# Kernel optimization log

Hardware: AMD Instinct MI355X
Metric: run time of the kernel (lower is better)

## Reference

```python
import jax, jax.numpy as jnp
import numpy as np

EPS = 1e-5


def setup_inputs() -> dict:
    key = jax.random.key(0)
    k1, k2, k3 = jax.random.split(key, 3)
    B, C, H, W = 32, 512, 56, 56
    R = 16
    x = jax.random.normal(k1, (B, C, H, W), dtype=jnp.float32)
    # SE excitation weights (no bias): Linear(C -> C//R), Linear(C//R -> C)
    w1 = jax.random.normal(k2, (C // R, C), dtype=jnp.float32) * (1.0 / np.sqrt(C))
    w2 = jax.random.normal(k3, (C, C // R), dtype=jnp.float32) * (1.0 / np.sqrt(C // R))
    # BatchNorm2d affine params (init: weight=1, bias=0)
    bn_weight = jnp.ones((C,), dtype=jnp.float32)
    bn_bias = jnp.zeros((C,), dtype=jnp.float32)
    return {"x": x, "w1": w1, "w2": w2, "bn_weight": bn_weight, "bn_bias": bn_bias}


def reference(x, w1, w2, bn_weight, bn_bias):
    B, C, H, W = x.shape
    # squeeze: global average pool -> [B, C]
    s = jnp.mean(x, axis=(2, 3))
    # excitation: Linear -> ReLU -> Linear -> Sigmoid
    e = jax.nn.sigmoid(jax.nn.relu(s @ w1.T) @ w2.T)  # [B, C]
    # scale
    y = x * e[:, :, None, None]  # [B, C, H, W]
    # BatchNorm2d (training-mode batch statistics, biased variance)
    mean = jnp.mean(y, axis=(0, 2, 3))
    var = jnp.var(y, axis=(0, 2, 3))
    yn = (y - mean[None, :, None, None]) * (
        bn_weight[None, :, None, None] * jax.lax.rsqrt(var + EPS)[None, :, None, None]
    ) + bn_bias[None, :, None, None]
    # unsqueeze dim=1 (c1=1) then rearrange 'b c1 (c2 c3) h w -> b c2 (c1 c3) h w', c2=2
    z = yn.reshape(B, 2, C // 2, H, W)
    # flatten(-2).mean(-1): mean over spatial dims -> [B, 2, C//2]
    z = jnp.mean(z, axis=(3, 4))
    # sum over dim=1 -> [B, C//2]
    return jnp.sum(z, axis=1)
```

## Files before the change

### kernel.cpp

```cpp
#include <hip/hip_runtime.h>
#include <math.h>

constexpr int B  = 32;
constexpr int C  = 512;
constexpr int CR = 32;
constexpr int HW = 56 * 56;
constexpr int NV4 = HW / 4;
constexpr float EPS = 1e-5f;

typedef float f32x4 __attribute__((ext_vector_type(4)));

__device__ inline f32x4 ntload(const f32x4* p) {
    return __builtin_nontemporal_load(p);
}

__global__ __launch_bounds__(256) void rowstats(const float* __restrict__ x,
                                                float* __restrict__ s_out,
                                                float* __restrict__ q_out) {
    const int wid  = threadIdx.x >> 6;
    const int lane = threadIdx.x & 63;
    const int row  = blockIdx.x * 4 + wid;
    const f32x4* xp = reinterpret_cast<const f32x4*>(x) + (size_t)row * NV4 + lane;
    float s = 0.f, q = 0.f;
    #pragma unroll
    for (int i = 0; i < 12; ++i) {
        f32x4 v = ntload(xp + i * 64);
        s += (v.x + v.y) + (v.z + v.w);
        q += (v.x * v.x + v.y * v.y) + (v.z * v.z + v.w * v.w);
    }
    {
        const float v = __builtin_nontemporal_load(x + (size_t)row * HW + 3072 + lane);
        s += v;
        q = fmaf(v, v, q);
    }
    #pragma unroll
    for (int off = 32; off > 0; off >>= 1) {
        s += __shfl_down(s, off, 64);
        q += __shfl_down(q, off, 64);
    }
    if (lane == 0) {
        s_out[row] = s * (1.0f / (float)HW);
        q_out[row] = q;
    }
}

__global__ __launch_bounds__(512) void excite(const float* __restrict__ s_in,
                                              const float* __restrict__ q_in,
                                              const float* __restrict__ w1,
                                              const float* __restrict__ w2,
                                              float* __restrict__ m_out,
                                              float* __restrict__ eq_out) {
    const int b   = blockIdx.x;
    const int tid = threadIdx.x;
    __shared__ __align__(16) float sh_s[C];
    __shared__ float sh_h[CR];

    const int j = tid >> 4, t = tid & 15;

    float4 w1r[8];
    {
        const float4* wr = reinterpret_cast<const float4*>(w1 + j * C);
        #pragma unroll
        for (int k = 0; k < 8; ++k) w1r[k] = wr[t + 16 * k];
    }
    float4 w2r[8];
    {
        const float4* w2p = reinterpret_cast<const float4*>(w2 + tid * CR);
        #pragma unroll
        for (int k = 0; k < 8; ++k) w2r[k] = w2p[k];
    }
    const float qv = q_in[b * C + tid];
    const float sv = s_in[b * C + tid];
    sh_s[tid] = sv;
    __syncthreads();

    {
        const float4* sr = reinterpret_cast<const float4*>(sh_s);
        float acc = 0.f;
        #pragma unroll
        for (int k = 0; k < 8; ++k) {
            float4 wv = w1r[k];
            float4 svv = sr[t + 16 * k];
            acc = fmaf(svv.x, wv.x, fmaf(svv.y, wv.y, fmaf(svv.z, wv.z, fmaf(svv.w, wv.w, acc))));
        }
        #pragma unroll
        for (int off = 8; off > 0; off >>= 1)
            acc += __shfl_down(acc, off, 16);
        if (t == 0) sh_h[j] = fmaxf(acc, 0.f);
    }
    __syncthreads();

    {
        const float4* hp = reinterpret_cast<const float4*>(sh_h);
        float acc = 0.f;
        #pragma unroll
        for (int k = 0; k < CR / 4; ++k) {
            float4 wv = w2r[k];
            float4 hv = hp[k];
            acc = fmaf(hv.x, wv.x, fmaf(hv.y, wv.y, fmaf(hv.z, wv.z, fmaf(hv.w, wv.w, acc))));
        }
        const float e = 1.0f / (1.0f + expf(-acc));
        m_out[b * C + tid]  = e * sv;
        eq_out[b * C + tid] = e * e * qv;
    }
}

__global__ __launch_bounds__(512) void bnout(const float* __restrict__ m_in,
                                             const float* __restrict__ eq_in,
                                             const float* __restrict__ bnw,
                                             const float* __restrict__ bnb,
                                             float* __restrict__ out) {
    const int c = threadIdx.x;
    __shared__ float sh_z[B][C / 2];
    const float wv = bnw[c];
    const float bv = bnb[c];
    float mv[B];
    float mean = 0.f, eq = 0.f;
    #pragma unroll
    for (int b = 0; b < B; ++b) {
        mv[b] = m_in[b * C + c];
        eq   += eq_in[b * C + c];
        mean += mv[b];
    }
    mean *= (1.0f / (float)B);
    const float var = eq * (1.0f / ((float)B * (float)HW)) - mean * mean;
    const float g   = wv * rsqrtf(var + EPS);

    if (c < C / 2) {
        #pragma unroll
        for (int b = 0; b < B; ++b)
            sh_z[b][c] = (mv[b] - mean) * g + bv;
    }
    __syncthreads();
    if (c >= C / 2) {
        const int c2 = c - C / 2;
        #pragma unroll
        for (int b = 0; b < B; ++b)
            out[b * (C / 2) + c2] = sh_z[b][c2] + ((mv[b] - mean) * g + bv);
    }
}

extern "C" void kernel_launch(void* const* d_in, const int* in_sizes, int n_in,
                              void* d_out, int out_size, void* d_ws, size_t ws_size,
                              hipStream_t stream) {
    const float* x   = (const float*)d_in[0];
    const float* w1  = (const float*)d_in[1];
    const float* w2  = (const float*)d_in[2];
    const float* bnw = (const float*)d_in[3];
    const float* bnb = (const float*)d_in[4];
    float* out = (float*)d_out;

    float* s_ws  = (float*)d_ws;
    float* q_ws  = s_ws + B * C;
    float* m_ws  = q_ws + B * C;
    float* eq_ws = m_ws + B * C;

    rowstats<<<dim3(B * C / 4), dim3(256), 0, stream>>>(x, s_ws, q_ws);
    excite<<<dim3(B), dim3(512), 0, stream>>>(s_ws, q_ws, w1, w2, m_ws, eq_ws);
    bnout<<<dim3(1), dim3(512), 0, stream>>>(m_ws, eq_ws, bnw, bnb, out);
}
```

Before: 40.31 us.

## Fuse excitation and batch-norm output kernels via cooperative grid sync

Measured after the change: 67.66 us. 1.68x slower.

```diff
diff --git a/kernel.cpp b/kernel.cpp
--- a/kernel.cpp
+++ b/kernel.cpp
@@ -1,5 +1,8 @@
 #include <hip/hip_runtime.h>
+#include <hip/hip_cooperative_groups.h>
 #include <math.h>
+
+namespace cg = cooperative_groups;
 
 constexpr int B  = 32;
 constexpr int C  = 512;
@@ -44,19 +47,22 @@
     }
 }
 
-__global__ __launch_bounds__(512) void excite(const float* __restrict__ s_in,
-                                              const float* __restrict__ q_in,
-                                              const float* __restrict__ w1,
-                                              const float* __restrict__ w2,
-                                              float* __restrict__ m_out,
-                                              float* __restrict__ eq_out) {
+__global__ __launch_bounds__(512) void excite_bn(const float* __restrict__ s_in,
+                                                 const float* __restrict__ q_in,
+                                                 const float* __restrict__ w1,
+                                                 const float* __restrict__ w2,
+                                                 const float* __restrict__ bnw,
+                                                 const float* __restrict__ bnb,
+                                                 float* __restrict__ m_ws,
+                                                 float* __restrict__ eq_ws,
+                                                 float* __restrict__ out) {
     const int b   = blockIdx.x;
     const int tid = threadIdx.x;
     __shared__ __align__(16) float sh_s[C];
     __shared__ float sh_h[CR];
+    __shared__ float sh_mean[16], sh_g[16], sh_bv[16];
 
     const int j = tid >> 4, t = tid & 15;
-
     float4 w1r[8];
     {
         const float4* wr = reinterpret_cast<const float4*>(w1 + j * C);
@@ -100,43 +106,45 @@
             acc = fmaf(hv.x, wv.x, fmaf(hv.y, wv.y, fmaf(hv.z, wv.z, fmaf(hv.w, wv.w, acc))));
         }
         const float e = 1.0f / (1.0f + expf(-acc));
-        m_out[b * C + tid]  = e * sv;
-        eq_out[b * C + tid] = e * e * qv;
+        m_ws[b * C + tid]  = e * sv;
+        eq_ws[b * C + tid] = e * e * qv;
     }
-}
 
-__global__ __launch_bounds__(512) void bnout(const float* __restrict__ m_in,
-                                             const float* __restrict__ eq_in,
-                                             const float* __restrict__ bnw,
-                                             const float* __restrict__ bnb,
-                                             float* __restrict__ out) {
-    const int c = threadIdx.x;
-    __shared__ float sh_z[B][C / 2];
-    const float wv = bnw[c];
-    const float bv = bnb[c];
-    float mv[B];
-    float mean = 0.f, eq = 0.f;
-    #pragma unroll
-    for (int b = 0; b < B; ++b) {
-        mv[b] = m_in[b * C + c];
-        eq   += eq_in[b * C + c];
-        mean += mv[b];
-    }
-    mean *= (1.0f / (float)B);
-    const float var = eq * (1.0f / ((float)B * (float)HW)) - mean * mean;
-    const float g   = wv * rsqrtf(var + EPS);
+    __threadfence();
+    cg::this_grid().sync();
 
-    if (c < C / 2) {
+    const int base = blockIdx.x * 8;
+    {
+        const int k  = tid >> 5;
+        const int bb = tid & 31;
+        const int chan = (k < 8) ? (base + k) : (C / 2 + base + (k - 8));
+        float mvv = m_ws[bb * C + chan];
+        float evv = eq_ws[bb * C + chan];
         #pragma unroll
-        for (int b = 0; b < B; ++b)
-            sh_z[b][c] = (mv[b] - mean) * g + bv;
+        for (int off = 16; off > 0; off >>= 1) {
+            mvv += __shfl_down(mvv, off, 32);
+            evv += __shfl_down(evv, off, 32);
+        }
+        if (bb == 0) {
+            const float mean = mvv * (1.0f / (float)B);
+            const float var  = evv * (1.0f / ((float)B * (float)HW)) - mean * mean;
+            sh_mean[k] = mean;
+            sh_g[k]    = bnw[chan] * rsqrtf(var + EPS);
+            sh_bv[k]   = bnb[chan];
+        }
     }
     __syncthreads();
-    if (c >= C / 2) {
-        const int c2 = c - C / 2;
-        #pragma unroll
-        for (int b = 0; b < B; ++b)
-            out[b * (C / 2) + c2] = sh_z[b][c2] + ((mv[b] - mean) * g + bv);
+
+    if (tid < 256) {
+        const int bb = tid & 31;
+        const int i  = tid >> 5;
+        const int ca = base + i;
+        const int cb = C / 2 + base + i;
+        const float ma = m_ws[bb * C + ca];
+        const float mb = m_ws[bb * C + cb];
+        out[bb * (C / 2) + ca] =
+            (ma - sh_mean[i])     * sh_g[i]     + sh_bv[i] +
+            (mb - sh_mean[i + 8]) * sh_g[i + 8] + sh_bv[i + 8];
     }
 }
 
@@ -156,6 +164,10 @@
     float* eq_ws = m_ws + B * C;
 
     rowstats<<<dim3(B * C / 4), dim3(256), 0, stream>>>(x, s_ws, q_ws);
-    excite<<<dim3(B), dim3(512), 0, stream>>>(s_ws, q_ws, w1, w2, m_ws, eq_ws);
-    bnout<<<dim3(1), dim3(512), 0, stream>>>(m_ws, eq_ws, bnw, bnb, out);
+
+    void* args[] = {(void*)&s_ws, (void*)&q_ws, (void*)&w1, (void*)&w2,
+                    (void*)&bnw, (void*)&bnb, (void*)&m_ws, (void*)&eq_ws,
+                    (void*)&out};
+    hipLaunchCooperativeKernel((const void*)excite_bn, dim3(B), dim3(512),
+                               args, 0, stream);
 }
```
